# Performance work log

Hardware: AMD Instinct MI355X
Metric: run time of the kernel (lower is better)

Reference implementation:

```python
import jax, jax.numpy as jnp
import numpy as np

GRID_SIZE = 8
IN_DIM = 1024
OUT_DIM = 1024
BATCH = 4096


def setup_inputs() -> dict:
    key = jax.random.key(0)
    k1, k2, k3 = jax.random.split(key, 3)
    noise_scale = 0.1
    noise_scale_base = 0.1
    x = jax.random.normal(k1, (BATCH, IN_DIM), dtype=jnp.float32)
    scale_base = (1.0 / np.sqrt(IN_DIM)
                  + (jax.random.normal(k2, (OUT_DIM, IN_DIM), dtype=jnp.float32) * 2 - 1)
                  * noise_scale_base)
    scale_spline = jnp.full((OUT_DIM, IN_DIM), 1.0, dtype=jnp.float32)
    coeff = (jax.random.uniform(k3, (2, OUT_DIM, IN_DIM, GRID_SIZE), dtype=jnp.float32)
             * noise_scale / (np.sqrt(IN_DIM) * np.sqrt(GRID_SIZE)))
    return {"x": x, "scale_base": scale_base, "scale_spline": scale_spline,
            "coeff": coeff}


def reference(x, scale_base, scale_spline, coeff):
    # x: (B, I); scale_base/scale_spline: (O, I); coeff: (2, O, I, G)
    G = coeff.shape[-1]
    k = jnp.arange(1, G + 1, dtype=x.dtype)          # (G,)
    ang = x[:, :, None] * k                           # (B, I, G)
    cos_b = jnp.cos(ang)
    sin_b = jnp.sin(ang)
    # fold scale_spline into coeff: (2, O, I, G)
    w = scale_spline[None, :, :, None] * coeff
    spline = (jnp.einsum('big,oig->bo', cos_b, w[0])
              + jnp.einsum('big,oig->bo', sin_b, w[1]))  # (B, O)
    base = jnp.einsum('bi,oi->bo', jax.nn.silu(x), scale_base)
    return base + spline
```

## Files before the change

### kernel.cpp

```cpp
#include <hip/hip_runtime.h>
#include <hip/hip_bf16.h>
#include <stdint.h>

#define BATCH   4096
#define IN_DIM  1024
#define OUT_DIM 1024
#define GRID_G  8
#define K8      16384
#define KB      1024
#define SPLIT8  4
#define WSCALE  256.0f

typedef __bf16 bf16x8 __attribute__((ext_vector_type(8)));
typedef __bf16 bf16x4 __attribute__((ext_vector_type(4)));
typedef float  f32x4  __attribute__((ext_vector_type(4)));
typedef int    i32x4  __attribute__((ext_vector_type(4)));
typedef int    i32x8  __attribute__((ext_vector_type(8)));

__global__ __launch_bounds__(256) void prep(const float* __restrict__ x,
                                            const float* __restrict__ sb,
                                            const float* __restrict__ ss,
                                            const float* __restrict__ coeff,
                                            uint8_t* __restrict__ A8,
                                            uint8_t* __restrict__ W8,
                                            __bf16* __restrict__ Ab,
                                            __bf16* __restrict__ Wb,
                                            float* __restrict__ C) {
    __shared__ __align__(16) float lds[8192];
    const int tid = threadIdx.x;

    if (blockIdx.x < 1024) {
        const int t  = blockIdx.x * 256 + tid;
        const int b  = t >> 6;
        const int i0 = (t & 63) * 16;

        {
            float4 z = make_float4(0.f, 0.f, 0.f, 0.f);
            float4* cz = (float4*)(C + (size_t)blockIdx.x * 4096);
#pragma unroll
            for (int j = 0; j < 4; ++j) cz[j * 256 + tid] = z;
        }

        float xv[16];
        {
            const float4* xp = (const float4*)(x + (size_t)b * IN_DIM + i0);
            float4 q0 = xp[0], q1 = xp[1], q2 = xp[2], q3 = xp[3];
            xv[0]=q0.x;  xv[1]=q0.y;  xv[2]=q0.z;  xv[3]=q0.w;
            xv[4]=q1.x;  xv[5]=q1.y;  xv[6]=q1.z;  xv[7]=q1.w;
            xv[8]=q2.x;  xv[9]=q2.y;  xv[10]=q2.z; xv[11]=q2.w;
            xv[12]=q3.x; xv[13]=q3.y; xv[14]=q3.z; xv[15]=q3.w;
        }

        float c1[16], s1[16], ck[16], sk[16];
        bf16x8 va, vb;
#pragma unroll
        for (int j = 0; j < 16; ++j) {
            float e  = __expf(-xv[j]);
            float sl = xv[j] * __builtin_amdgcn_rcpf(1.f + e);
            if (j < 8) va[j & 7] = (__bf16)sl; else vb[j & 7] = (__bf16)sl;
            s1[j] = __sinf(xv[j]);
            c1[j] = __cosf(xv[j]);
            ck[j] = c1[j]; sk[j] = s1[j];
        }
        *(bf16x8*)(Ab + (size_t)b * IN_DIM + i0)     = va;
        *(bf16x8*)(Ab + (size_t)b * IN_DIM + i0 + 8) = vb;

        uint8_t* a8 = A8 + (size_t)b * K8 + i0;
#pragma unroll
        for (int g = 0; g < GRID_G; ++g) {
            i32x4 wc, ws;
#pragma unroll
            for (int q = 0; q < 4; ++q) {
                int dc = 0, ds = 0;
                dc = __builtin_amdgcn_cvt_pk_fp8_f32(ck[4*q+0], ck[4*q+1], dc, false);
                dc = __builtin_amdgcn_cvt_pk_fp8_f32(ck[4*q+2], ck[4*q+3], dc, true);
                ds = __builtin_amdgcn_cvt_pk_fp8_f32(sk[4*q+0], sk[4*q+1], ds, false);
                ds = __builtin_amdgcn_cvt_pk_fp8_f32(sk[4*q+2], sk[4*q+3], ds, true);
                wc[q] = dc; ws[q] = ds;
            }
            *(i32x4*)(a8 + (size_t)g * IN_DIM)            = wc;
            *(i32x4*)(a8 + (size_t)(GRID_G + g) * IN_DIM) = ws;
            if (g < GRID_G - 1) {
#pragma unroll
                for (int j = 0; j < 16; ++j) {
                    float cn = ck[j] * c1[j] - sk[j] * s1[j];
                    float sn = sk[j] * c1[j] + ck[j] * s1[j];
                    ck[j] = cn; sk[j] = sn;
                }
            }
        }
    } else {
        const int o   = blockIdx.x - 1024;
        const int i0  = tid * 4;
        const size_t oi = (size_t)o * IN_DIM + i0;

        const float4 s4 = *(const float4*)(ss + oi);
        const float  s[4] = {s4.x * WSCALE, s4.y * WSCALE, s4.z * WSCALE, s4.w * WSCALE};

        {
            float4 b4 = *(const float4*)(sb + oi);
            bf16x4 wv;
            wv[0] = (__bf16)b4.x; wv[1] = (__bf16)b4.y;
            wv[2] = (__bf16)b4.z; wv[3] = (__bf16)b4.w;
            *(bf16x4*)(Wb + oi) = wv;
        }

        uint8_t* w8 = W8 + (size_t)o * K8 + i0;
        for (int p = 0; p < 2; ++p) {
            if (p) __syncthreads();
            const float4* src = (const float4*)(coeff + ((size_t)p * OUT_DIM + o) * (IN_DIM * GRID_G));
#pragma unroll
            for (int j = 0; j < 8; ++j) {
                float4 v = src[j * 256 + tid];
                const int L   = j * 4096 + tid * 16;
                const int row = L >> 7;
                const int ch  = (L >> 4) & 7;
                *(float4*)((uint8_t*)lds + row * 128 + ((ch ^ (row & 7)) << 4)) = v;
            }
            __syncthreads();
            float c[4][8];
            {
                const uint8_t* rp = (const uint8_t*)lds + tid * 128;
                const int r7 = (tid & 7) << 4;
#pragma unroll
                for (int j = 0; j < 8; ++j) {
                    float4 v = *(const float4*)(rp + ((j << 4) ^ r7));
                    c[j >> 1][(j & 1) * 4 + 0] = v.x;
                    c[j >> 1][(j & 1) * 4 + 1] = v.y;
                    c[j >> 1][(j & 1) * 4 + 2] = v.z;
                    c[j >> 1][(j & 1) * 4 + 3] = v.w;
                }
            }
#pragma unroll
            for (int g = 0; g < GRID_G; ++g) {
                int d = 0;
                d = __builtin_amdgcn_cvt_pk_fp8_f32(s[0]*c[0][g], s[1]*c[1][g], d, false);
                d = __builtin_amdgcn_cvt_pk_fp8_f32(s[2]*c[2][g], s[3]*c[3][g], d, true);
                *(int*)(w8 + (size_t)(p * GRID_G + g) * IN_DIM) = d;
            }
        }
    }
}

__global__ __launch_bounds__(256, 4) void gemm_all(const uint8_t* __restrict__ A8,
                                                   const uint8_t* __restrict__ W8,
                                                   const uint8_t* __restrict__ Ab,
                                                   const uint8_t* __restrict__ Wb,
                                                   float* __restrict__ C) {
    __shared__ __align__(16) uint8_t As[16384];
    __shared__ __align__(16) uint8_t Bs[16384];
    const int tid = threadIdx.x;
    const int w   = tid >> 6;
    const int l   = tid & 63;
    const int flat = blockIdx.y * 8 + blockIdx.x;
    const int xcd  = flat & 7;
    const int idx  = flat >> 3;
    const int bn   = (xcd & 1) * 4 + (idx & 3);
    const int bm   = (xcd >> 1) * 8 + (idx >> 2);
    const int kz  = blockIdx.z;
    const int wm  = w & 1;
    const int wn  = w >> 1;

    f32x4 acc[4][4] = {};

    const int srow   = l >> 3;
    const int schunk = ((l & 7) ^ srow) * 16;
    const int lm = l & 15;
    const int q  = l >> 4;

    {
        const uint8_t* Ag = A8 + (size_t)(bm * 128 + w * 32 + srow) * K8 + kz * (K8 / SPLIT8) + schunk;
        const uint8_t* Bg = W8 + (size_t)(bn * 128 + w * 32 + srow) * K8 + kz * (K8 / SPLIT8) + schunk;
        const int c0 = (q * 2) << 4, c1 = (q * 2 + 1) << 4;

        for (int ks = 0; ks < (K8 / SPLIT8) / 128; ++ks) {
#pragma unroll
            for (int j = 0; j < 4; ++j) {
                __builtin_amdgcn_global_load_lds(
                    (const uint32_t*)(Ag + (size_t)(j * 8) * K8),
                    (uint32_t*)(As + (w * 32 + j * 8) * 128), 16, 0, 0);
                __builtin_amdgcn_global_load_lds(
                    (const uint32_t*)(Bg + (size_t)(j * 8) * K8),
                    (uint32_t*)(Bs + (w * 32 + j * 8) * 128), 16, 0, 0);
            }
            Ag += 128; Bg += 128;
            __syncthreads();

            i32x8 bf[4];
#pragma unroll
            for (int j = 0; j < 4; ++j) {
                const int row = wn * 64 + j * 16 + lm;
                const int sw  = (row & 7) << 4;
                const uint8_t* rp = Bs + row * 128;
                i32x4 lo = *(const i32x4*)(rp + (c0 ^ sw));
                i32x4 hi = *(const i32x4*)(rp + (c1 ^ sw));
                bf[j] = __builtin_shufflevector(lo, hi, 0, 1, 2, 3, 4, 5, 6, 7);
            }
#pragma unroll
            for (int i = 0; i < 4; ++i) {
                const int row = wm * 64 + i * 16 + lm;
                const int sw  = (row & 7) << 4;
                const uint8_t* rp = As + row * 128;
                i32x4 lo = *(const i32x4*)(rp + (c0 ^ sw));
                i32x4 hi = *(const i32x4*)(rp + (c1 ^ sw));
                i32x8 af = __builtin_shufflevector(lo, hi, 0, 1, 2, 3, 4, 5, 6, 7);
#pragma unroll
                for (int j = 0; j < 4; ++j)
                    acc[i][j] = __builtin_amdgcn_mfma_scale_f32_16x16x128_f8f6f4(
                        af, bf[j], acc[i][j], 0, 0, 0, 0x7f7f7f7f, 0, 0x7f7f7f7f);
            }
            __syncthreads();
        }
    }

#pragma unroll
    for (int i = 0; i < 4; ++i)
#pragma unroll
        for (int j = 0; j < 4; ++j)
            acc[i][j] *= (1.0f / WSCALE);

    {
        const uint8_t* Ag = Ab + (size_t)(bm * 128 + w * 32 + srow) * (KB * 2) + kz * 512 + schunk;
        const uint8_t* Bg = Wb + (size_t)(bn * 128 + w * 32 + srow) * (KB * 2) + kz * 512 + schunk;

        for (int ks = 0; ks < 4; ++ks) {
#pragma unroll
            for (int j = 0; j < 4; ++j) {
                __builtin_amdgcn_global_load_lds(
                    (const uint32_t*)(Ag + (size_t)(j * 8) * (KB * 2)),
                    (uint32_t*)(As + (w * 32 + j * 8) * 128), 16, 0, 0);
                __builtin_amdgcn_global_load_lds(
                    (const uint32_t*)(Bg + (size_t)(j * 8) * (KB * 2)),
                    (uint32_t*)(Bs + (w * 32 + j * 8) * 128), 16, 0, 0);
            }
            Ag += 128; Bg += 128;
            __syncthreads();

#pragma unroll
            for (int h = 0; h < 2; ++h) {
                bf16x8 af[4], bfr[4];
#pragma unroll
                for (int i = 0; i < 4; ++i) {
                    const int row = wm * 64 + i * 16 + lm;
                    af[i] = *(const bf16x8*)(As + row * 128 + ((((h * 4 + q) ^ (row & 7))) << 4));
                }
#pragma unroll
                for (int j = 0; j < 4; ++j) {
                    const int row = wn * 64 + j * 16 + lm;
                    bfr[j] = *(const bf16x8*)(Bs + row * 128 + ((((h * 4 + q) ^ (row & 7))) << 4));
                }
#pragma unroll
                for (int i = 0; i < 4; ++i)
#pragma unroll
                    for (int j = 0; j < 4; ++j)
                        acc[i][j] = __builtin_amdgcn_mfma_f32_16x16x32_bf16(af[i], bfr[j], acc[i][j], 0, 0, 0);
            }
            __syncthreads();
        }
    }

    const int row0 = bm * 128 + wm * 64 + q * 4;
    const int col0 = bn * 128 + wn * 64 + lm;
#pragma unroll
    for (int i = 0; i < 4; ++i)
#pragma unroll
        for (int j = 0; j < 4; ++j)
#pragma unroll
            for (int r = 0; r < 4; ++r)
                unsafeAtomicAdd(&C[(size_t)(row0 + i * 16 + r) * OUT_DIM + col0 + j * 16],
                                acc[i][j][r]);
}

extern "C" void kernel_launch(void* const* d_in, const int* in_sizes, int n_in,
                              void* d_out, int out_size, void* d_ws, size_t ws_size,
                              hipStream_t stream) {
    const float* x     = (const float*)d_in[0];
    const float* sb    = (const float*)d_in[1];
    const float* ss    = (const float*)d_in[2];
    const float* coeff = (const float*)d_in[3];
    float* out = (float*)d_out;

    uint8_t* A8 = (uint8_t*)d_ws;
    uint8_t* W8 = A8 + (size_t)BATCH * K8;
    __bf16*  Ab = (__bf16*)(W8 + (size_t)OUT_DIM * K8);
    __bf16*  Wb = Ab + (size_t)BATCH * KB;

    hipLaunchKernelGGL(prep, dim3(2048), dim3(256), 0, stream,
                       x, sb, ss, coeff, A8, W8, Ab, Wb, out);
    hipLaunchKernelGGL(gemm_all, dim3(OUT_DIM / 128, BATCH / 128, SPLIT8), dim3(256), 0, stream,
                       A8, W8, (const uint8_t*)Ab, (const uint8_t*)Wb, out);
}
```

Measured before the change: 235.0 us.

## Use nontemporal loads/stores in prep and split GEMM K into two launches

Prep kernel loads and stores now use nontemporal hints, so the streamed x/coeff reads and A8/W8 writes avoid cache pollution. The split-K GEMM is cut into 8 K-chunks run as two sequential launches of 4 chunks each, so each block covers half the previous K range. The second launch may get cached tiles while the first drains, and each block's wave is shorter. This adds a launch and doubles the atomic or partial accumulations into C, and the nontemporal stores may hurt reuse of A8/W8 by the GEMM.

Result: slower. 318.9 us (+35.7%).

```diff
diff --git a/kernel.cpp b/kernel.cpp
--- a/kernel.cpp
+++ b/kernel.cpp
@@ -8,7 +8,7 @@
 #define GRID_G  8
 #define K8      16384
 #define KB      1024
-#define SPLIT8  4
+#define NCHUNK  8
 #define WSCALE  256.0f
 
 typedef __bf16 bf16x8 __attribute__((ext_vector_type(8)));
@@ -43,12 +43,18 @@
 
         float xv[16];
         {
-            const float4* xp = (const float4*)(x + (size_t)b * IN_DIM + i0);
-            float4 q0 = xp[0], q1 = xp[1], q2 = xp[2], q3 = xp[3];
-            xv[0]=q0.x;  xv[1]=q0.y;  xv[2]=q0.z;  xv[3]=q0.w;
-            xv[4]=q1.x;  xv[5]=q1.y;  xv[6]=q1.z;  xv[7]=q1.w;
-            xv[8]=q2.x;  xv[9]=q2.y;  xv[10]=q2.z; xv[11]=q2.w;
-            xv[12]=q3.x; xv[13]=q3.y; xv[14]=q3.z; xv[15]=q3.w;
+            const f32x4* xp = (const f32x4*)(x + (size_t)b * IN_DIM + i0);
+            f32x4 q0 = __builtin_nontemporal_load(xp + 0);
+            f32x4 q1 = __builtin_nontemporal_load(xp + 1);
+            f32x4 q2 = __builtin_nontemporal_load(xp + 2);
+            f32x4 q3 = __builtin_nontemporal_load(xp + 3);
+#pragma unroll
+            for (int j = 0; j < 4; ++j) {
+                xv[j]      = q0[j];
+                xv[4 + j]  = q1[j];
+                xv[8 + j]  = q2[j];
+                xv[12 + j] = q3[j];
+            }
         }
 
         float c1[16], s1[16], ck[16], sk[16];
@@ -62,8 +68,8 @@
             c1[j] = __cosf(xv[j]);
             ck[j] = c1[j]; sk[j] = s1[j];
         }
-        *(bf16x8*)(Ab + (size_t)b * IN_DIM + i0)     = va;
-        *(bf16x8*)(Ab + (size_t)b * IN_DIM + i0 + 8) = vb;
+        __builtin_nontemporal_store(va, (bf16x8*)(Ab + (size_t)b * IN_DIM + i0));
+        __builtin_nontemporal_store(vb, (bf16x8*)(Ab + (size_t)b * IN_DIM + i0 + 8));
 
         uint8_t* a8 = A8 + (size_t)b * K8 + i0;
 #pragma unroll
@@ -78,8 +84,8 @@
                 ds = __builtin_amdgcn_cvt_pk_fp8_f32(sk[4*q+2], sk[4*q+3], ds, true);
                 wc[q] = dc; ws[q] = ds;
             }
-            *(i32x4*)(a8 + (size_t)g * IN_DIM)            = wc;
-            *(i32x4*)(a8 + (size_t)(GRID_G + g) * IN_DIM) = ws;
+            __builtin_nontemporal_store(wc, (i32x4*)(a8 + (size_t)g * IN_DIM));
+            __builtin_nontemporal_store(ws, (i32x4*)(a8 + (size_t)(GRID_G + g) * IN_DIM));
             if (g < GRID_G - 1) {
 #pragma unroll
                 for (int j = 0; j < 16; ++j) {
@@ -94,28 +100,28 @@
         const int i0  = tid * 4;
         const size_t oi = (size_t)o * IN_DIM + i0;
 
-        const float4 s4 = *(const float4*)(ss + oi);
-        const float  s[4] = {s4.x * WSCALE, s4.y * WSCALE, s4.z * WSCALE, s4.w * WSCALE};
+        const f32x4 s4 = __builtin_nontemporal_load((const f32x4*)(ss + oi));
+        const float  s[4] = {s4[0] * WSCALE, s4[1] * WSCALE, s4[2] * WSCALE, s4[3] * WSCALE};
 
         {
-            float4 b4 = *(const float4*)(sb + oi);
+            f32x4 b4 = __builtin_nontemporal_load((const f32x4*)(sb + oi));
             bf16x4 wv;
-            wv[0] = (__bf16)b4.x; wv[1] = (__bf16)b4.y;
-            wv[2] = (__bf16)b4.z; wv[3] = (__bf16)b4.w;
-            *(bf16x4*)(Wb + oi) = wv;
+            wv[0] = (__bf16)b4[0]; wv[1] = (__bf16)b4[1];
+            wv[2] = (__bf16)b4[2]; wv[3] = (__bf16)b4[3];
+            __builtin_nontemporal_store(wv, (bf16x4*)(Wb + oi));
         }
 
         uint8_t* w8 = W8 + (size_t)o * K8 + i0;
         for (int p = 0; p < 2; ++p) {
             if (p) __syncthreads();
-            const float4* src = (const float4*)(coeff + ((size_t)p * OUT_DIM + o) * (IN_DIM * GRID_G));
+            const f32x4* src = (const f32x4*)(coeff + ((size_t)p * OUT_DIM + o) * (IN_DIM * GRID_G));
 #pragma unroll
             for (int j = 0; j < 8; ++j) {
-                float4 v = src[j * 256 + tid];
+                f32x4 v = __builtin_nontemporal_load(src + j * 256 + tid);
                 const int L   = j * 4096 + tid * 16;
                 const int row = L >> 7;
                 const int ch  = (L >> 4) & 7;
-                *(float4*)((uint8_t*)lds + row * 128 + ((ch ^ (row & 7)) << 4)) = v;
+                *(f32x4*)((uint8_t*)lds + row * 128 + ((ch ^ (row & 7)) << 4)) = v;
             }
             __syncthreads();
             float c[4][8];
@@ -124,11 +130,11 @@
                 const int r7 = (tid & 7) << 4;
 #pragma unroll
                 for (int j = 0; j < 8; ++j) {
-                    float4 v = *(const float4*)(rp + ((j << 4) ^ r7));
-                    c[j >> 1][(j & 1) * 4 + 0] = v.x;
-                    c[j >> 1][(j & 1) * 4 + 1] = v.y;
-                    c[j >> 1][(j & 1) * 4 + 2] = v.z;
-                    c[j >> 1][(j & 1) * 4 + 3] = v.w;
+                    f32x4 v = *(const f32x4*)(rp + ((j << 4) ^ r7));
+                    c[j >> 1][(j & 1) * 4 + 0] = v[0];
+                    c[j >> 1][(j & 1) * 4 + 1] = v[1];
+                    c[j >> 1][(j & 1) * 4 + 2] = v[2];
+                    c[j >> 1][(j & 1) * 4 + 3] = v[3];
                 }
             }
 #pragma unroll
@@ -136,7 +142,7 @@
                 int d = 0;
                 d = __builtin_amdgcn_cvt_pk_fp8_f32(s[0]*c[0][g], s[1]*c[1][g], d, false);
                 d = __builtin_amdgcn_cvt_pk_fp8_f32(s[2]*c[2][g], s[3]*c[3][g], d, true);
-                *(int*)(w8 + (size_t)(p * GRID_G + g) * IN_DIM) = d;
+                __builtin_nontemporal_store(d, (int*)(w8 + (size_t)(p * GRID_G + g) * IN_DIM));
             }
         }
     }
@@ -146,7 +152,8 @@
                                                    const uint8_t* __restrict__ W8,
                                                    const uint8_t* __restrict__ Ab,
                                                    const uint8_t* __restrict__ Wb,
-                                                   float* __restrict__ C) {
+                                                   float* __restrict__ C,
+                                                   int kz0) {
     __shared__ __align__(16) uint8_t As[16384];
     __shared__ __align__(16) uint8_t Bs[16384];
     const int tid = threadIdx.x;
@@ -157,7 +164,7 @@
     const int idx  = flat >> 3;
     const int bn   = (xcd & 1) * 4 + (idx & 3);
     const int bm   = (xcd >> 1) * 8 + (idx >> 2);
-    const int kz  = blockIdx.z;
+    const int kz  = kz0 + blockIdx.z;
     const int wm  = w & 1;
     const int wn  = w >> 1;
 
@@ -169,11 +176,11 @@
     const int q  = l >> 4;
 
     {
-        const uint8_t* Ag = A8 + (size_t)(bm * 128 + w * 32 + srow) * K8 + kz * (K8 / SPLIT8) + schunk;
-        const uint8_t* Bg = W8 + (size_t)(bn * 128 + w * 32 + srow) * K8 + kz * (K8 / SPLIT8) + schunk;
+        const uint8_t* Ag = A8 + (size_t)(bm * 128 + w * 32 + srow) * K8 + kz * (K8 / NCHUNK) + schunk;
+        const uint8_t* Bg = W8 + (size_t)(bn * 128 + w * 32 + srow) * K8 + kz * (K8 / NCHUNK) + schunk;
         const int c0 = (q * 2) << 4, c1 = (q * 2 + 1) << 4;
 
-        for (int ks = 0; ks < (K8 / SPLIT8) / 128; ++ks) {
+        for (int ks = 0; ks < (K8 / NCHUNK) / 128; ++ks) {
 #pragma unroll
             for (int j = 0; j < 4; ++j) {
                 __builtin_amdgcn_global_load_lds(
@@ -220,10 +227,10 @@
             acc[i][j] *= (1.0f / WSCALE);
 
     {
-        const uint8_t* Ag = Ab + (size_t)(bm * 128 + w * 32 + srow) * (KB * 2) + kz * 512 + schunk;
-        const uint8_t* Bg = Wb + (size_t)(bn * 128 + w * 32 + srow) * (KB * 2) + kz * 512 + schunk;
-
-        for (int ks = 0; ks < 4; ++ks) {
+        const uint8_t* Ag = Ab + (size_t)(bm * 128 + w * 32 + srow) * (KB * 2) + kz * 256 + schunk;
+        const uint8_t* Bg = Wb + (size_t)(bn * 128 + w * 32 + srow) * (KB * 2) + kz * 256 + schunk;
+
+        for (int ks = 0; ks < 2; ++ks) {
 #pragma unroll
             for (int j = 0; j < 4; ++j) {
                 __builtin_amdgcn_global_load_lds(
@@ -287,6 +294,8 @@
 
     hipLaunchKernelGGL(prep, dim3(2048), dim3(256), 0, stream,
                        x, sb, ss, coeff, A8, W8, Ab, Wb, out);
-    hipLaunchKernelGGL(gemm_all, dim3(OUT_DIM / 128, BATCH / 128, SPLIT8), dim3(256), 0, stream,
-                       A8, W8, (const uint8_t*)Ab, (const uint8_t*)Wb, out);
+    hipLaunchKernelGGL(gemm_all, dim3(OUT_DIM / 128, BATCH / 128, NCHUNK / 2), dim3(256), 0, stream,
+                       A8, W8, (const uint8_t*)Ab, (const uint8_t*)Wb, out, 0);
+    hipLaunchKernelGGL(gemm_all, dim3(OUT_DIM / 128, BATCH / 128, NCHUNK / 2), dim3(256), 0, stream,
+                       A8, W8, (const uint8_t*)Ab, (const uint8_t*)Wb, out, 4);
 }
```
